# Kernel optimization log

Hardware: AMD Instinct MI355X
Metric: run time of the kernel (lower is better)

## Reference

```python
import jax, jax.numpy as jnp
import numpy as np

T, B, D = 512, 16, 512
H, DH, DI, L = 8, 64, 2048, 4
EPS = 1e-6
SCALE = 1.0 / DH ** 0.5
NEG_INF = -1e9


def _ln(x, g, b):
    m = jnp.mean(x, axis=-1, keepdims=True)
    v = jnp.var(x, axis=-1, keepdims=True)
    return (x - m) * jax.lax.rsqrt(v + EPS) * g + b


def _pos_emb(pos_seq):
    inv_freq = 1.0 / (10000.0 ** (jnp.arange(0, D, 2, dtype=jnp.float32) / D))
    s = pos_seq[:, None] * inv_freq[None, :]  # (rlen, D/2)
    return jnp.concatenate([jnp.sin(s), jnp.cos(s)], axis=-1)  # (rlen, D)


def _rel_shift(x, klen):
    # faithful reshape-slice trick: (q, r, b, n) -> view as (r, q, b, n), drop first, back to (q, r-1, b, n)
    q, r, b, n = x.shape
    x = x.reshape(r, q, b, n)[1:].reshape(q, r - 1, b, n)
    return x[:, :klen]


def _layer(h, r, r_w_bias, r_r_bias, attn_mask, qkv_w, r_net_w, o_w,
           ln1_g, ln1_b, w1, b1, w2, b2, ln2_g, ln2_b):
    qlen, bsz, _ = h.shape
    rlen = r.shape[0]
    w_heads = jnp.einsum('ibd,de->ibe', h, qkv_w)
    q, k, v = jnp.split(w_heads, 3, axis=-1)
    q = q.reshape(qlen, bsz, H, DH)
    k = k.reshape(qlen, bsz, H, DH)
    v = v.reshape(qlen, bsz, H, DH)
    rk = jnp.einsum('jbd,de->jbe', r, r_net_w).reshape(rlen, bsz, H, DH)
    AC = jnp.einsum('ibnd,jbnd->ijbn', q + r_w_bias, k)
    BD = _rel_shift(jnp.einsum('ibnd,jbnd->ijbn', q + r_r_bias, rk), qlen)
    score = (AC + BD) * SCALE
    score = jnp.where(attn_mask[None, :, :, None], NEG_INF, score)
    prob = jax.nn.softmax(score, axis=1)
    vec = jnp.einsum('ijbn,jbnd->ibnd', prob, v).reshape(qlen, bsz, H * DH)
    out = _ln(h + jnp.einsum('ibe,ed->ibd', vec, o_w), ln1_g, ln1_b)
    ff = jnp.maximum(jnp.einsum('ibd,df->ibf', out, w1) + b1, 0.0)
    ff = jnp.einsum('ibf,fd->ibd', ff, w2) + b2
    return _ln(out + ff, ln2_g, ln2_b)


def setup_inputs() -> dict:
    key = jax.random.key(0)
    ks = jax.random.split(key, 12)
    s = 0.02
    lengths = jax.random.randint(ks[0], (B,), T // 2, T + 1)
    seq_mask = jnp.arange(T)[None, :] < lengths[:, None]  # (B, T) bool, True = real token
    return {
        'h': jax.random.normal(ks[1], (B, T, D), jnp.float32),
        'seq_mask': seq_mask,
        'r_w_bias': jax.random.normal(ks[2], (H, DH), jnp.float32) * s,
        'r_r_bias': jax.random.normal(ks[3], (H, DH), jnp.float32) * s,
        'top_ln_g': jnp.ones((D,), jnp.float32),
        'top_ln_b': jnp.zeros((D,), jnp.float32),
        'qkv_w': jax.random.normal(ks[4], (L, D, 3 * H * DH), jnp.float32) * s,
        'r_net_w': jax.random.normal(ks[5], (L, D, H * DH), jnp.float32) * s,
        'o_w': jax.random.normal(ks[6], (L, H * DH, D), jnp.float32) * s,
        'attn_ln_g': jnp.ones((L, D), jnp.float32),
        'attn_ln_b': jnp.zeros((L, D), jnp.float32),
        'ff_w1': jax.random.normal(ks[7], (L, D, DI), jnp.float32) * s,
        'ff_b1': jnp.zeros((L, DI), jnp.float32),
        'ff_w2': jax.random.normal(ks[8], (L, DI, D), jnp.float32) * s,
        'ff_b2': jnp.zeros((L, D), jnp.float32),
        'ff_ln_g': jnp.ones((L, D), jnp.float32),
        'ff_ln_b': jnp.zeros((L, D), jnp.float32),
    }


def reference(h, seq_mask, r_w_bias, r_r_bias, top_ln_g, top_ln_b, qkv_w, r_net_w, o_w,
              attn_ln_g, attn_ln_b, ff_w1, ff_b1, ff_w2, ff_b2, ff_ln_g, ff_ln_b):
    h = jnp.transpose(h, (1, 0, 2))            # (T, B, D)
    attn_mask = ~jnp.transpose(seq_mask, (1, 0))  # (T, B), True = padding
    fw = _pos_emb(jnp.arange(T, -T, -1, dtype=h.dtype))
    bw = _pos_emb(jnp.arange(-T, T, 1, dtype=h.dtype))
    pos = jnp.concatenate([
        jnp.broadcast_to(fw[:, None, :], (2 * T, B // 2, D)),
        jnp.broadcast_to(bw[:, None, :], (2 * T, B - B // 2, D)),
    ], axis=1)                                 # (2T, B, D)
    h = _ln(h, top_ln_g, top_ln_b)
    hids = [h]
    out = h
    for i in range(L):
        out = _layer(out, pos, r_w_bias, r_r_bias, attn_mask,
                     qkv_w[i], r_net_w[i], o_w[i], attn_ln_g[i], attn_ln_b[i],
                     ff_w1[i], ff_b1[i], ff_w2[i], ff_b2[i], ff_ln_g[i], ff_ln_b[i])
        hids.append(out)
    out = jnp.transpose(out, (1, 0, 2))
    hids = tuple(jnp.transpose(x, (1, 0, 2)) for x in hids)
    return (out, hids)
```

## Files before the change

kernel.cpp:

```cpp
#include <hip/hip_runtime.h>
#include <cstddef>


typedef unsigned short u16;
typedef short s16x8 __attribute__((ext_vector_type(8)));
typedef unsigned short u16x8 __attribute__((ext_vector_type(8)));
typedef float f32x4 __attribute__((ext_vector_type(4)));

__device__ __forceinline__ u16 f2bf(float f) {
  unsigned int u = __float_as_uint(f);
  u += 0x7fffu + ((u >> 16) & 1u);
  return (u16)(u >> 16);
}
__device__ __forceinline__ float bf2f(u16 u) {
  return __uint_as_float((unsigned int)u << 16);
}

__device__ __forceinline__ f32x4 mfma16(s16x8 a, s16x8 b, f32x4 c) {
  return __builtin_amdgcn_mfma_f32_16x16x32_bf16(a, b, c, 0, 0, 0);
}

__device__ __forceinline__ void gl2lds16(const u16* g, u16* l) {
  __builtin_amdgcn_global_load_lds(
      (const __attribute__((address_space(1))) unsigned int*)g,
      (__attribute__((address_space(3))) unsigned int*)l, 16, 0, 0);
}

template <int MODE, int TN>
__launch_bounds__(256) __global__
void gemm_bt(const u16* __restrict__ A, const u16* __restrict__ Bt,
             int M, int N, int K,
             void* p0, void* p1, void* p2, void* p3,
             const float* __restrict__ p4, const float* __restrict__ p5) {
  (void)M;
  constexpr int NT = TN / 32;
  __shared__ u16 As[4096];
  __shared__ u16 Bs[TN * 32];
  const int tid = threadIdx.x;
  const int lane = tid & 63;
  const int w = tid >> 6;
  const int quad = lane >> 4, l15 = lane & 15;
  const int m0 = blockIdx.y << 7, n0 = blockIdx.x * TN;

  if constexpr (MODE == 0) {
    A += (size_t)blockIdx.z * 524288;
    p0 = (void*)((u16*)p0 + (size_t)blockIdx.z * 524288);
  }

  f32x4 acc[4][NT];
#pragma unroll
  for (int a = 0; a < 4; ++a)
#pragma unroll
    for (int b = 0; b < NT; ++b) {
      f32x4 z = {0.f, 0.f, 0.f, 0.f};
      acc[a][b] = z;
    }

  const int slot0 = w * 64 + lane;
  const int rA = slot0 >> 2, cA = (slot0 & 3) * 8;
  const u16* gA0 = A + (size_t)(m0 + rA) * K + cA;
  const u16* gA1 = A + (size_t)(m0 + 64 + rA) * K + cA;
  const u16* gB0 = Bt + (size_t)(n0 + rA) * K + cA;
  const u16* gB1 = Bt + (size_t)(n0 + 64 + rA) * K + cA;
  u16* lA0 = &As[w * 512];
  u16* lA1 = &As[(4 + w) * 512];
  u16* lB0 = &Bs[w * 512];
  u16* lB1 = &Bs[(4 + w) * 512];

  const int wm = (w >> 1) << 6, wn = (w & 1) * (NT * 16);
  const int nk = K >> 5;
  for (int kt = 0; kt < nk; ++kt) {
    const int k0 = kt << 5;
    gl2lds16(gA0 + k0, lA0);
    gl2lds16(gA1 + k0, lA1);
    gl2lds16(gB0 + k0, lB0);
    if constexpr (TN == 128) gl2lds16(gB1 + k0, lB1);
    __syncthreads();
    s16x8 af[4], bfg[NT];
#pragma unroll
    for (int t = 0; t < 4; ++t)
      af[t] = *(const s16x8*)&As[(wm + t * 16 + l15) * 32 + quad * 8];
#pragma unroll
    for (int t = 0; t < NT; ++t)
      bfg[t] = *(const s16x8*)&Bs[(wn + t * 16 + l15) * 32 + quad * 8];
#pragma unroll
    for (int mt = 0; mt < 4; ++mt)
#pragma unroll
      for (int nt = 0; nt < NT; ++nt)
        acc[mt][nt] = mfma16(af[mt], bfg[nt], acc[mt][nt]);
    __syncthreads();
  }

#pragma unroll
  for (int mt = 0; mt < 4; ++mt) {
#pragma unroll
    for (int nt = 0; nt < NT; ++nt) {
#pragma unroll
      for (int r = 0; r < 4; ++r) {
        const int row = m0 + wm + mt * 16 + quad * 4 + r;
        const int col = n0 + wn + nt * 16 + l15;
        const float v = acc[mt][nt][r];
        if constexpr (MODE == 0) {
          const int hn = col >> 6, d = col & 63;
          ((u16*)p0)[((size_t)hn * 1024 + row) * 64 + d] = f2bf(v);
        } else if constexpr (MODE == 1) {
          const int i = row >> 4, b = row & 15;
          const int which = col >> 9, hn = (col >> 6) & 7, d = col & 63;
          const int bn = b * 8 + hn;
          const size_t idx = ((size_t)bn * 512 + i) * 64 + d;
          if (which == 0) {
            ((u16*)p0)[idx] = f2bf(v + p4[hn * 64 + d]);
            ((u16*)p1)[idx] = f2bf(v + p5[hn * 64 + d]);
          } else if (which == 1) {
            ((u16*)p2)[idx] = f2bf(v);
          } else {
            ((u16*)p3)[idx] = f2bf(v);
          }
        } else if constexpr (MODE == 2) {
          ((float*)p0)[(size_t)row * N + col] =
              v + ((const float*)p1)[(size_t)row * N + col];
        } else if constexpr (MODE == 3) {
          ((float*)p0)[(size_t)row * N + col] =
              v + ((const float*)p1)[(size_t)row * N + col] +
              ((const float*)p2)[col];
        } else {
          float t = v + ((const float*)p1)[col];
          ((u16*)p0)[(size_t)row * N + col] = f2bf(t > 0.f ? t : 0.f);
        }
      }
    }
  }
}

__launch_bounds__(256) __global__
void transpose_w_kernel(const float* __restrict__ qkv, const float* __restrict__ rnet,
                        const float* __restrict__ ow, const float* __restrict__ w1,
                        const float* __restrict__ w2, u16* __restrict__ dst) {
  const int type = blockIdx.z, l = blockIdx.y, tile = blockIdx.x;
  int R, C;
  const float* src;
  u16* out;
  switch (type) {
    case 0: R = 512; C = 1536; src = qkv + (size_t)l * 786432; out = dst + (size_t)l * 786432; break;
    case 1: R = 512; C = 512;  src = rnet + (size_t)l * 262144; out = dst + 3145728 + (size_t)l * 262144; break;
    case 2: R = 512; C = 512;  src = ow + (size_t)l * 262144;   out = dst + 4194304 + (size_t)l * 262144; break;
    case 3: R = 512; C = 2048; src = w1 + (size_t)l * 1048576;  out = dst + 5242880 + (size_t)l * 1048576; break;
    default: R = 2048; C = 512; src = w2 + (size_t)l * 1048576; out = dst + 9437184 + (size_t)l * 1048576; break;
  }
  const int tC = C >> 6;
  const int tR = R >> 6;
  if (tile >= tC * tR) return;
  const int r0 = (tile / tC) << 6, c0 = (tile % tC) << 6;
  __shared__ float tb[64][65];
  const int tid = threadIdx.x;
  const int rr = tid >> 2, cc = (tid & 3) << 4;
#pragma unroll
  for (int j = 0; j < 4; ++j) {
    f32x4 u = *(const f32x4*)(src + (size_t)(r0 + rr) * C + c0 + cc + j * 4);
    tb[rr][cc + j * 4 + 0] = u[0];
    tb[rr][cc + j * 4 + 1] = u[1];
    tb[rr][cc + j * 4 + 2] = u[2];
    tb[rr][cc + j * 4 + 3] = u[3];
  }
  __syncthreads();
  u16x8 o0, o1;
#pragma unroll
  for (int j = 0; j < 8; ++j) o0[j] = f2bf(tb[cc + j][rr]);
#pragma unroll
  for (int j = 0; j < 8; ++j) o1[j] = f2bf(tb[cc + 8 + j][rr]);
  *(u16x8*)(out + (size_t)(c0 + rr) * R + r0 + cc) = o0;
  *(u16x8*)(out + (size_t)(c0 + rr) * R + r0 + cc + 8) = o1;
}

__launch_bounds__(256) __global__
void posemb_kernel(u16* __restrict__ r_bf) {
  const int idx = blockIdx.x * 256 + threadIdx.x;
  const int d = idx & 511, j = (idx >> 9) & 1023, g = idx >> 19;
  const float pos = g ? (float)(j - 512) : (float)(512 - j);
  const int dp = d & 255;
  const float invf = expf((float)dp * (-9.210340371976184f / 256.f));
  const float v = pos * invf;
  r_bf[idx] = f2bf((d < 256) ? sinf(v) : cosf(v));
}

__launch_bounds__(256) __global__
void transpose_v_kernel(const u16* __restrict__ Vb, u16* __restrict__ Vt) {
  const int bn = blockIdx.y, j0 = blockIdx.x << 6;
  __shared__ u16 tb[64][72];
  const int tid = threadIdx.x;
#pragma unroll
  for (int q = 0; q < 2; ++q) {
    const int s = q * 256 + tid;
    const int jj = s >> 3, c = s & 7;
    u16x8 u = *(const u16x8*)(Vb + ((size_t)bn * 512 + j0 + jj) * 64 + c * 8);
    *(u16x8*)&tb[jj][c * 8] = u;
  }
  __syncthreads();
#pragma unroll
  for (int q = 0; q < 2; ++q) {
    const int s = q * 256 + tid;
    const int d = s >> 3, c = s & 7;
    u16x8 o;
#pragma unroll
    for (int e = 0; e < 8; ++e) o[e] = tb[c * 8 + e][d];
    *(u16x8*)(Vt + ((size_t)bn * 64 + d) * 512 + j0 + c * 8) = o;
  }
}

__launch_bounds__(256) __global__
void attn_kernel(const u16* __restrict__ Qw, const u16* __restrict__ Qr,
                 const u16* __restrict__ Kb, const u16* __restrict__ Vt,
                 const u16* __restrict__ rkb, const int* __restrict__ smask,
                 u16* __restrict__ vecb) {
  __shared__ u16 Ks[4096];
  __shared__ u16 Vts[4096];
  __shared__ u16 Band[8192];
  __shared__ u16 Ps[4096];

  const int tid = threadIdx.x, lane = tid & 63, w = tid >> 6;
  const int quad = lane >> 4, l15 = lane & 15;
  const int bn = blockIdx.x, b = bn >> 3, n = bn & 7;
  const int g = (b >= 8) ? 1 : 0;
  const int i0 = blockIdx.y << 6;

  unsigned mbits = 0;
  const int* smb = smask + b * 512 + l15;
#pragma unroll
  for (int s = 0; s < 32; ++s)
    if (smb[s * 16]) mbits |= 1u << s;
  unsigned vmask = 0;
#pragma unroll
  for (int jt = 0; jt < 8; ++jt)
    if (__any((int)((mbits >> (jt * 4)) & 15u))) vmask |= 1u << jt;
  const int ntiles = vmask ? (32 - __clz((int)vmask)) : 0;

  const u16* qwp = Qw + ((size_t)bn * 512 + i0 + w * 16 + l15) * 64 + quad * 8;
  const u16* qrp = Qr + ((size_t)bn * 512 + i0 + w * 16 + l15) * 64 + quad * 8;
  const s16x8 qw0 = *(const s16x8*)qwp, qw1 = *(const s16x8*)(qwp + 32);
  const s16x8 qr0 = *(const s16x8*)qrp, qr1 = *(const s16x8*)(qrp + 32);

  const u16* kbase = Kb + (size_t)bn * (512 * 64);
  const u16* vbase = Vt + (size_t)bn * (64 * 512);
  const u16* rkg = rkb + (size_t)(g * 8 + n) * (1024 * 64);

  const int s0 = w * 64 + lane;
  const int rl = s0 >> 3;
  const int cd = ((s0 & 7) ^ (rl & 7)) * 8;
  u16* lK0 = &Ks[w * 512];
  u16* lK1 = &Ks[(4 + w) * 512];
  u16* lV0 = &Vts[w * 512];
  u16* lV1 = &Vts[(4 + w) * 512];
  u16* lBq[4] = {&Band[w * 512], &Band[(4 + w) * 512], &Band[(8 + w) * 512],
                 &Band[(12 + w) * 512]};
  u16* pwv = &Ps[w * 1024];

  const int sw8 = ((quad ^ (l15 & 7)) * 8);
  const int sw8b = (((quad ^ (l15 & 7)) ^ 4) * 8);

  int sl[4], hisel[4];
#pragma unroll
  for (int r = 0; r < 4; ++r) {
    const int e = 15 + l15 - quad * 4 - r;
    sl[r] = (quad << 4) | (e & 15);
    hisel[r] = e >> 4;
  }

  f32x4 O[4];
  float m_st[4], l_st[4];
#pragma unroll
  for (int t = 0; t < 4; ++t) {
    f32x4 z = {0.f, 0.f, 0.f, 0.f};
    O[t] = z;
    m_st[t] = -1e30f;
    l_st[t] = 0.f;
  }

  for (int jt = 0; jt < ntiles; ++jt) {
    const int j0 = jt << 6;
    const int jr0 = 449 + j0 - i0;
    __syncthreads();
    gl2lds16(kbase + (size_t)(j0 + rl) * 64 + cd, lK0);
    gl2lds16(kbase + (size_t)(j0 + 32 + rl) * 64 + cd, lK1);
    gl2lds16(vbase + (size_t)rl * 512 + j0 + cd, lV0);
    gl2lds16(vbase + (size_t)(rl + 32) * 512 + j0 + cd, lV1);
    if (jt == 0) {
#pragma unroll
      for (int q = 0; q < 4; ++q) {
        int rrow = jr0 + q * 32 + rl;
        rrow = rrow < 1023 ? rrow : 1023;
        gl2lds16(rkg + (size_t)rrow * 64 + cd, lBq[q]);
      }
    } else {
      const int segb = ((jt + 1) & 1) << 1;
#pragma unroll
      for (int q = 0; q < 2; ++q) {
        int rrow = jr0 + 64 + q * 32 + rl;
        rrow = rrow < 1023 ? rrow : 1023;
        gl2lds16(rkg + (size_t)rrow * 64 + cd, lBq[segb + q]);
      }
    }
    __syncthreads();

    f32x4 ac[4];
#pragma unroll
    for (int t = 0; t < 4; ++t) {
      f32x4 z = {0.f, 0.f, 0.f, 0.f};
      ac[t] = z;
      s16x8 k0f = *(const s16x8*)&Ks[(t * 16 + l15) * 64 + sw8];
      s16x8 k1f = *(const s16x8*)&Ks[(t * 16 + l15) * 64 + sw8b];
      ac[t] = mfma16(qw0, k0f, ac[t]);
      ac[t] = mfma16(qw1, k1f, ac[t]);
    }
    const int bb0 = 48 - w * 16;
    const int rofs = (jt & 1) << 6;
    f32x4 bd[5];
#pragma unroll
    for (int t = 0; t < 5; ++t) {
      f32x4 z = {0.f, 0.f, 0.f, 0.f};
      const int prow = ((bb0 + t * 16 + l15) + rofs) & 127;
      s16x8 b0f = *(const s16x8*)&Band[prow * 64 + sw8];
      s16x8 b1f = *(const s16x8*)&Band[prow * 64 + sw8b];
      bd[t] = mfma16(qr1, b1f, mfma16(qr0, b0f, z));
    }
    float sh[5][4];
#pragma unroll
    for (int t = 0; t < 5; ++t)
#pragma unroll
      for (int r = 0; r < 4; ++r) sh[t][r] = __shfl(bd[t][r], sl[r]);

    float pv[4][4];
#pragma unroll
    for (int t = 0; t < 4; ++t) {
      const float mk = ((mbits >> (jt * 4 + t)) & 1u) ? 0.f : -1e9f;
#pragma unroll
      for (int r = 0; r < 4; ++r) {
        const float bdv = hisel[r] ? sh[t + 1][r] : sh[t][r];
        pv[t][r] = (ac[t][r] + bdv) * 0.125f + mk;
      }
    }
#pragma unroll
    for (int r = 0; r < 4; ++r) {
      float mx = fmaxf(fmaxf(pv[0][r], pv[1][r]), fmaxf(pv[2][r], pv[3][r]));
#pragma unroll
      for (int xm = 1; xm < 16; xm <<= 1) mx = fmaxf(mx, __shfl_xor(mx, xm));
      const float mn = fmaxf(m_st[r], mx);
      const float al = __expf(m_st[r] - mn);
      m_st[r] = mn;
      float rs = 0.f;
#pragma unroll
      for (int t = 0; t < 4; ++t) {
        pv[t][r] = __expf(pv[t][r] - mn);
        rs += pv[t][r];
      }
#pragma unroll
      for (int xm = 1; xm < 16; xm <<= 1) rs += __shfl_xor(rs, xm);
      l_st[r] = l_st[r] * al + rs;
#pragma unroll
      for (int t = 0; t < 4; ++t) O[t][r] *= al;
    }
#pragma unroll
    for (int t = 0; t < 4; ++t)
#pragma unroll
      for (int r = 0; r < 4; ++r) {
        const int row = quad * 4 + r, col = t * 16 + l15;
        pwv[row * 64 + ((((col >> 3) ^ row) & 7) << 3) + (col & 7)] =
            f2bf(pv[t][r]);
      }
#pragma unroll
    for (int ks = 0; ks < 2; ++ks) {
      const int ch = (((ks * 4 + quad) ^ l15) & 7) << 3;
      s16x8 pf = *(const s16x8*)&pwv[l15 * 64 + ch];
#pragma unroll
      for (int td = 0; td < 4; ++td) {
        s16x8 vf = *(const s16x8*)&Vts[(td * 16 + l15) * 64 +
                                       (ks == 0 ? sw8 : sw8b)];
        O[td] = mfma16(pf, vf, O[td]);
      }
    }
  }

#pragma unroll
  for (int td = 0; td < 4; ++td) {
#pragma unroll
    for (int r = 0; r < 4; ++r) {
      const int i = i0 + w * 16 + quad * 4 + r;
      const float val = O[td][r] / l_st[r];
      vecb[((size_t)i * 16 + b) * 512 + n * 64 + td * 16 + l15] = f2bf(val);
    }
  }
}

__launch_bounds__(256) __global__
void ln_kernel(const float* __restrict__ src, int src_is_bt,
               const float* __restrict__ gw, const float* __restrict__ bww,
               float* __restrict__ dst32, u16* __restrict__ dstbf,
               float* __restrict__ o1, float* __restrict__ o2) {
  const int row = blockIdx.x * 4 + (threadIdx.x >> 6);
  const int lane = threadIdx.x & 63;
  const int i = row >> 4, b = row & 15;
  const float* x = src + (src_is_bt ? ((size_t)b * 512 + i) * 512 : (size_t)row * 512);
  f32x4 u0 = *(const f32x4*)(x + lane * 8);
  f32x4 u1 = *(const f32x4*)(x + lane * 8 + 4);
  float s = u0[0] + u0[1] + u0[2] + u0[3] + u1[0] + u1[1] + u1[2] + u1[3];
  float sq = u0[0] * u0[0] + u0[1] * u0[1] + u0[2] * u0[2] + u0[3] * u0[3] +
             u1[0] * u1[0] + u1[1] * u1[1] + u1[2] * u1[2] + u1[3] * u1[3];
  for (int m = 1; m < 64; m <<= 1) {
    s += __shfl_xor(s, m);
    sq += __shfl_xor(sq, m);
  }
  const float mean = s * (1.f / 512.f);
  const float var = sq * (1.f / 512.f) - mean * mean;
  const float rs = rsqrtf(var + 1e-6f);
  f32x4 g0 = *(const f32x4*)(gw + lane * 8);
  f32x4 g1 = *(const f32x4*)(gw + lane * 8 + 4);
  f32x4 b0 = *(const f32x4*)(bww + lane * 8);
  f32x4 b1 = *(const f32x4*)(bww + lane * 8 + 4);
  f32x4 y0, y1;
#pragma unroll
  for (int k = 0; k < 4; ++k) {
    y0[k] = (u0[k] - mean) * rs * g0[k] + b0[k];
    y1[k] = (u1[k] - mean) * rs * g1[k] + b1[k];
  }
  const size_t o_ib = (size_t)row * 512 + lane * 8;
  const size_t o_tb = ((size_t)b * 512 + i) * 512 + lane * 8;
  if (dst32) {
    *(f32x4*)(dst32 + o_ib) = y0;
    *(f32x4*)(dst32 + o_ib + 4) = y1;
  }
  if (dstbf) {
    u16x8 ov;
#pragma unroll
    for (int k = 0; k < 4; ++k) {
      ov[k] = f2bf(y0[k]);
      ov[k + 4] = f2bf(y1[k]);
    }
    *(u16x8*)(dstbf + o_ib) = ov;
  }
  if (o1) {
    *(f32x4*)(o1 + o_tb) = y0;
    *(f32x4*)(o1 + o_tb + 4) = y1;
  }
  if (o2) {
    *(f32x4*)(o2 + o_tb) = y0;
    *(f32x4*)(o2 + o_tb + 4) = y1;
  }
}

extern "C" void kernel_launch(void* const* d_in, const int* in_sizes, int n_in,
                              void* d_out, int out_size, void* d_ws, size_t ws_size,
                              hipStream_t stream) {
  (void)in_sizes; (void)n_in; (void)out_size; (void)ws_size;
  const float* h_in = (const float*)d_in[0];
  const int* smask = (const int*)d_in[1];
  const float* rwb = (const float*)d_in[2];
  const float* rrb = (const float*)d_in[3];
  const float* top_g = (const float*)d_in[4];
  const float* top_b = (const float*)d_in[5];
  const float* qkv_w = (const float*)d_in[6];
  const float* rnet_w = (const float*)d_in[7];
  const float* o_w = (const float*)d_in[8];
  const float* attn_g = (const float*)d_in[9];
  const float* attn_b = (const float*)d_in[10];
  const float* w1 = (const float*)d_in[11];
  const float* b1 = (const float*)d_in[12];
  const float* w2 = (const float*)d_in[13];
  const float* b2 = (const float*)d_in[14];
  const float* ff_g = (const float*)d_in[15];
  const float* ff_b = (const float*)d_in[16];
  float* out = (float*)d_out;
  const size_t BTD = 4194304;

  char* ws = (char*)d_ws;
  size_t off = 0;
  auto alloc = [&](size_t bytes) {
    void* p = ws + off;
    off += (bytes + 255) & ~(size_t)255;
    return p;
  };
  u16* wT = (u16*)alloc(13631488ull * 2);
  u16* r_bf = (u16*)alloc(2ull * 1024 * 512 * 2);
  u16* rkb = (u16*)alloc(2ull * 8 * 1024 * 64 * 2);
  u16* Qw = (u16*)alloc(8ull << 20);
  u16* Qr = (u16*)alloc(8ull << 20);
  u16* Kb = (u16*)alloc(8ull << 20);
  u16* Vt = (u16*)alloc(8ull << 20);
  u16* vecb = (u16*)alloc(8ull << 20);
  u16* Xbf = (u16*)alloc(8ull << 20);
  u16* ffbf = (u16*)alloc(32ull << 20);
  float* hcur = (float*)alloc(16ull << 20);
  float* tmp = (float*)Qw;
  float* mid = (float*)Kb;
  u16* Vb = ffbf;

  dim3 blk(256);
  transpose_w_kernel<<<dim3(256, 4, 5), blk, 0, stream>>>(qkv_w, rnet_w, o_w, w1, w2, wT);
  posemb_kernel<<<dim3(4096), blk, 0, stream>>>(r_bf);
  ln_kernel<<<dim3(2048), blk, 0, stream>>>(h_in, 1, top_g, top_b, hcur, Xbf,
                                            out + BTD, (float*)nullptr);

  for (int l = 0; l < 4; ++l) {
    u16* qkvT = wT + (size_t)l * 786432;
    u16* rnetT = wT + 3145728 + (size_t)l * 262144;
    u16* oT = wT + 4194304 + (size_t)l * 262144;
    u16* w1T = wT + 5242880 + (size_t)l * 1048576;
    u16* w2T = wT + 9437184 + (size_t)l * 1048576;

    gemm_bt<0, 64><<<dim3(8, 8, 2), blk, 0, stream>>>(
        r_bf, rnetT, 1024, 512, 512,
        rkb, nullptr, nullptr, nullptr, nullptr, nullptr);

    gemm_bt<1, 128><<<dim3(12, 64), blk, 0, stream>>>(
        Xbf, qkvT, 8192, 1536, 512, Qw, Qr, Kb, Vb, rwb, rrb);

    transpose_v_kernel<<<dim3(8, 128), blk, 0, stream>>>(Vb, Vt);

    attn_kernel<<<dim3(128, 8), blk, 0, stream>>>(Qw, Qr, Kb, Vt, rkb, smask, vecb);

    gemm_bt<2, 64><<<dim3(8, 64), blk, 0, stream>>>(
        vecb, oT, 8192, 512, 512, tmp, hcur, nullptr, nullptr, nullptr, nullptr);

    ln_kernel<<<dim3(2048), blk, 0, stream>>>(tmp, 0, attn_g + l * 512, attn_b + l * 512,
                                              mid, Xbf, (float*)nullptr, (float*)nullptr);

    gemm_bt<4, 128><<<dim3(16, 64), blk, 0, stream>>>(
        Xbf, w1T, 8192, 2048, 512, ffbf, (void*)(b1 + (size_t)l * 2048),
        nullptr, nullptr, nullptr, nullptr);

    gemm_bt<3, 64><<<dim3(8, 64), blk, 0, stream>>>(
        ffbf, w2T, 8192, 512, 2048, tmp, mid, (void*)(b2 + (size_t)l * 512),
        nullptr, nullptr, nullptr);

    ln_kernel<<<dim3(2048), blk, 0, stream>>>(
        tmp, 0, ff_g + l * 512, ff_b + l * 512, hcur, Xbf,
        out + (size_t)(2 + l) * BTD, (l == 3) ? out : (float*)nullptr);
  }
}
```

Baseline: 1.110 ms.

## Register-prefetch next attention K/V/rk tile to overlap loads with compute

Replaces the per-iteration direct global-to-LDS loads with a software pipeline. The next tile's K, V and relative-key rows are loaded into registers while the current tile is computed, then written to LDS after a barrier, with hand-placed waitcnt and barriers. It also adds a minimum-occupancy hint to launch bounds. The goal is to hide global load latency behind MFMA work. In exchange it uses more registers, and the manual synchronization could be fragile.

```diff
diff --git a/kernel.cpp b/kernel.cpp
--- a/kernel.cpp
+++ b/kernel.cpp
@@ -207,7 +207,14 @@
   }
 }
 
-__launch_bounds__(256) __global__
+#define ATTN_FENCE_BAR()                                    \
+  do {                                                      \
+    asm volatile("s_waitcnt lgkmcnt(0)" ::: "memory");      \
+    __builtin_amdgcn_s_barrier();                           \
+    __builtin_amdgcn_sched_barrier(0);                      \
+  } while (0)
+
+__launch_bounds__(256, 4) __global__
 void attn_kernel(const u16* __restrict__ Qw, const u16* __restrict__ Qr,
                  const u16* __restrict__ Kb, const u16* __restrict__ Vt,
                  const u16* __restrict__ rkb, const int* __restrict__ smask,
@@ -275,31 +282,58 @@
     l_st[t] = 0.f;
   }
 
+  s16x8 rK0, rK1, rV0, rV1, rB0, rB1;
+  auto issue_prefetch = [&](int nt) {
+    const int j0n = nt << 6;
+    const int jr0n = 449 + j0n - i0;
+    rK0 = *(const s16x8*)(kbase + (size_t)(j0n + rl) * 64 + cd);
+    rK1 = *(const s16x8*)(kbase + (size_t)(j0n + 32 + rl) * 64 + cd);
+    rV0 = *(const s16x8*)(vbase + (size_t)rl * 512 + j0n + cd);
+    rV1 = *(const s16x8*)(vbase + (size_t)(rl + 32) * 512 + j0n + cd);
+    int rr0 = jr0n + 64 + rl;
+    int rr1 = jr0n + 96 + rl;
+    rr0 = rr0 < 1023 ? rr0 : 1023;
+    rr1 = rr1 < 1023 ? rr1 : 1023;
+    rB0 = *(const s16x8*)(rkg + (size_t)rr0 * 64 + cd);
+    rB1 = *(const s16x8*)(rkg + (size_t)rr1 * 64 + cd);
+  };
+
   for (int jt = 0; jt < ntiles; ++jt) {
     const int j0 = jt << 6;
-    const int jr0 = 449 + j0 - i0;
-    __syncthreads();
-    gl2lds16(kbase + (size_t)(j0 + rl) * 64 + cd, lK0);
-    gl2lds16(kbase + (size_t)(j0 + 32 + rl) * 64 + cd, lK1);
-    gl2lds16(vbase + (size_t)rl * 512 + j0 + cd, lV0);
-    gl2lds16(vbase + (size_t)(rl + 32) * 512 + j0 + cd, lV1);
     if (jt == 0) {
+      const int jr00 = 449 - i0;
+      gl2lds16(kbase + (size_t)rl * 64 + cd, lK0);
+      gl2lds16(kbase + (size_t)(32 + rl) * 64 + cd, lK1);
+      gl2lds16(vbase + (size_t)rl * 512 + cd, lV0);
+      gl2lds16(vbase + (size_t)(rl + 32) * 512 + cd, lV1);
 #pragma unroll
       for (int q = 0; q < 4; ++q) {
-        int rrow = jr0 + q * 32 + rl;
+        int rrow = jr00 + q * 32 + rl;
         rrow = rrow < 1023 ? rrow : 1023;
         gl2lds16(rkg + (size_t)rrow * 64 + cd, lBq[q]);
       }
+      asm volatile("" ::: "memory");
+      __builtin_amdgcn_sched_barrier(0);
+      if (ntiles > 1) {
+        issue_prefetch(1);
+        asm volatile("s_waitcnt vmcnt(6)" ::: "memory");
+      } else {
+        asm volatile("s_waitcnt vmcnt(0)" ::: "memory");
+      }
+      __builtin_amdgcn_s_barrier();
+      __builtin_amdgcn_sched_barrier(0);
     } else {
+      ATTN_FENCE_BAR();
+      *(s16x8*)(lK0 + lane * 8) = rK0;
+      *(s16x8*)(lK1 + lane * 8) = rK1;
+      *(s16x8*)(lV0 + lane * 8) = rV0;
+      *(s16x8*)(lV1 + lane * 8) = rV1;
       const int segb = ((jt + 1) & 1) << 1;
-#pragma unroll
-      for (int q = 0; q < 2; ++q) {
-        int rrow = jr0 + 64 + q * 32 + rl;
-        rrow = rrow < 1023 ? rrow : 1023;
-        gl2lds16(rkg + (size_t)rrow * 64 + cd, lBq[segb + q]);
-      }
-    }
-    __syncthreads();
+      *(s16x8*)(lBq[segb] + lane * 8) = rB0;
+      *(s16x8*)(lBq[segb + 1] + lane * 8) = rB1;
+      if (jt + 1 < ntiles) issue_prefetch(jt + 1);
+      ATTN_FENCE_BAR();
+    }
 
     f32x4 ac[4];
 #pragma unroll
```

New measurement: 1.257 ms. 1.13x slower.

## Double GEMM K-tile to 64 and XOR-swizzle LDS layout

Applied to the files above, without the earlier changes.

The GEMM mainloop now stages a 64-wide K slice per iteration instead of 32, which halves the number of barrier pairs per output tile. Global-to-LDS loads use an XOR swizzle on the 16-byte column chunk, and fragment reads undo it, so the 128-byte LDS rows avoid bank conflicts. LDS use per block doubles, which may reduce occupancy. There is still no double buffering, so loads and MFMA work do not overlap.

```diff
diff --git a/kernel.cpp b/kernel.cpp
--- a/kernel.cpp
+++ b/kernel.cpp
@@ -34,8 +34,9 @@
              const float* __restrict__ p4, const float* __restrict__ p5) {
   (void)M;
   constexpr int NT = TN / 32;
-  __shared__ u16 As[4096];
-  __shared__ u16 Bs[TN * 32];
+  constexpr int NBQ = TN / 32;
+  __shared__ u16 As[128 * 64];
+  __shared__ u16 Bs[TN * 64];
   const int tid = threadIdx.x;
   const int lane = tid & 63;
   const int w = tid >> 6;
@@ -56,38 +57,41 @@
       acc[a][b] = z;
     }
 
-  const int slot0 = w * 64 + lane;
-  const int rA = slot0 >> 2, cA = (slot0 & 3) * 8;
-  const u16* gA0 = A + (size_t)(m0 + rA) * K + cA;
-  const u16* gA1 = A + (size_t)(m0 + 64 + rA) * K + cA;
-  const u16* gB0 = Bt + (size_t)(n0 + rA) * K + cA;
-  const u16* gB1 = Bt + (size_t)(n0 + 64 + rA) * K + cA;
-  u16* lA0 = &As[w * 512];
-  u16* lA1 = &As[(4 + w) * 512];
-  u16* lB0 = &Bs[w * 512];
-  u16* lB1 = &Bs[(4 + w) * 512];
+  const int rg = lane >> 3;
+  const int cz = ((lane & 7) ^ rg) << 3;
+  const u16* gA = A + (size_t)(m0 + w * 8 + rg) * K + cz;
+  const u16* gB = Bt + (size_t)(n0 + w * 8 + rg) * K + cz;
+  u16* lA = &As[w * 512];
+  u16* lB = &Bs[w * 512];
 
   const int wm = (w >> 1) << 6, wn = (w & 1) * (NT * 16);
-  const int nk = K >> 5;
+  const int rsw = l15 & 7;
+  const int nk = K >> 6;
   for (int kt = 0; kt < nk; ++kt) {
-    const int k0 = kt << 5;
-    gl2lds16(gA0 + k0, lA0);
-    gl2lds16(gA1 + k0, lA1);
-    gl2lds16(gB0 + k0, lB0);
-    if constexpr (TN == 128) gl2lds16(gB1 + k0, lB1);
+    const int k0 = kt << 6;
+#pragma unroll
+    for (int q = 0; q < 4; ++q)
+      gl2lds16(gA + (size_t)(q * 32) * K + k0, lA + q * 2048);
+#pragma unroll
+    for (int q = 0; q < NBQ; ++q)
+      gl2lds16(gB + (size_t)(q * 32) * K + k0, lB + q * 2048);
     __syncthreads();
-    s16x8 af[4], bfg[NT];
-#pragma unroll
-    for (int t = 0; t < 4; ++t)
-      af[t] = *(const s16x8*)&As[(wm + t * 16 + l15) * 32 + quad * 8];
-#pragma unroll
-    for (int t = 0; t < NT; ++t)
-      bfg[t] = *(const s16x8*)&Bs[(wn + t * 16 + l15) * 32 + quad * 8];
-#pragma unroll
-    for (int mt = 0; mt < 4; ++mt)
-#pragma unroll
-      for (int nt = 0; nt < NT; ++nt)
-        acc[mt][nt] = mfma16(af[mt], bfg[nt], acc[mt][nt]);
+#pragma unroll
+    for (int ks = 0; ks < 2; ++ks) {
+      const int co = ((ks * 4 + quad) ^ rsw) << 3;
+      s16x8 af[4], bfg[NT];
+#pragma unroll
+      for (int t = 0; t < 4; ++t)
+        af[t] = *(const s16x8*)&As[(wm + t * 16 + l15) * 64 + co];
+#pragma unroll
+      for (int t = 0; t < NT; ++t)
+        bfg[t] = *(const s16x8*)&Bs[(wn + t * 16 + l15) * 64 + co];
+#pragma unroll
+      for (int mt = 0; mt < 4; ++mt)
+#pragma unroll
+        for (int nt = 0; nt < NT; ++nt)
+          acc[mt][nt] = mfma16(af[mt], bfg[nt], acc[mt][nt]);
+    }
     __syncthreads();
   }
 
```

After: 1.070 ms. -3.6%, faster.
